# Kernel optimization log

Hardware: AMD Instinct MI355X
Metric: run time of the kernel (lower is better)

## Reference

```python
import jax, jax.numpy as jnp
import numpy as np

N_CLASSES = 19
N_BINS = 10
EPS = 1e-13


def setup_inputs() -> dict:
    key = jax.random.key(0)
    k1, k2 = jax.random.split(key)
    output = jax.random.normal(k1, (1, N_CLASSES, 1024, 2048), dtype=jnp.float32)
    target = jax.random.randint(k2, (1, 1024, 2048), 0, N_CLASSES, dtype=jnp.int32)
    return {"output": output, "target": target}


def reference(output, target):
    # output: [B, C, H, W] logits; target: [B, H, W] int labels
    B, C, H, W = output.shape
    p = jax.nn.softmax(output, axis=1)  # [B, C, H, W]

    # Bin i covers (i/N_BINS, (i+1)/N_BINS]; p == 0 belongs to no bin.
    bin_idx = jnp.clip(jnp.ceil(p * N_BINS).astype(jnp.int32) - 1, 0, N_BINS - 1)
    valid = p > 0

    cls = jnp.arange(C, dtype=jnp.int32)[None, :, None, None]  # idealMap per class
    # Combined (class, bin) segment id; invalid pixels dumped into extra segment.
    seg = jnp.where(valid, cls * N_BINS + bin_idx, C * N_BINS).reshape(-1)
    n_seg = C * N_BINS + 1

    p_flat = p.reshape(-1)
    conf_sum = jax.ops.segment_sum(p_flat, seg, num_segments=n_seg)[:-1].reshape(C, N_BINS)
    no_pred = jax.ops.segment_sum(jnp.ones_like(p_flat), seg, num_segments=n_seg)[:-1].reshape(C, N_BINS)
    correct = (target[:, None, :, :] == cls).astype(p.dtype)  # idealMap == target
    no_acc = jax.ops.segment_sum(correct.reshape(-1), seg, num_segments=n_seg)[:-1].reshape(C, N_BINS)

    avg_acc = no_acc / (no_pred + EPS)
    avg_conf = conf_sum / (no_pred + EPS)
    loss = jnp.sum((avg_acc - avg_conf) ** 2 * (no_pred / jnp.sum(no_pred)))
    return loss
```

## Files before the change

### kernel.cpp

```cpp
#include <hip/hip_runtime.h>

#define NC 19
#define NB 10
#define NCELL (NC * NB)
#define NPART (3 * NCELL + 2 * NC)
#define REP 4
#define NSLOT 16
#define BLOCKS 2048
#define TPB 256

__global__ __launch_bounds__(TPB) void cce_pass1(
    const float* __restrict__ logits, const int* __restrict__ tgt,
    float* __restrict__ gacc, int hw)
{
    constexpr int O_CONF = 0;
    constexpr int O_PRED = REP * NCELL;
    constexpr int O_ACC  = 2 * REP * NCELL;
    constexpr int O_PSUM = 3 * REP * NCELL;
    constexpr int O_INV  = 3 * REP * NCELL + REP * NC;
    constexpr int LDS_N  = O_INV + NC;

    __shared__ float lds[LDS_N];
    for (int i = threadIdx.x; i < LDS_N; i += TPB) lds[i] = 0.0f;
    __syncthreads();

    const int rep = threadIdx.x & (REP - 1);
    float psum[NC];
#pragma unroll
    for (int c = 0; c < NC; ++c) psum[c] = 0.0f;

    const int ngroups  = hw >> 1;
    const int tid      = blockIdx.x * TPB + threadIdx.x;
    const int nthreads = gridDim.x * TPB;

    for (int g = tid; g < ngroups; g += nthreads) {
        float xa[NC], xb[NC];
#pragma unroll
        for (int c = 0; c < NC; ++c) {
            const float2 v = *reinterpret_cast<const float2*>(
                logits + (size_t)c * hw + 2 * (size_t)g);
            xa[c] = v.x; xb[c] = v.y;
        }
        const int2 t2 = *reinterpret_cast<const int2*>(tgt + 2 * (size_t)g);

        float m0 = xa[0], m1 = xb[0];
#pragma unroll
        for (int c = 1; c < NC; ++c) { m0 = fmaxf(m0, xa[c]); m1 = fmaxf(m1, xb[c]); }

        float s0 = 0.0f, s1 = 0.0f;
#pragma unroll
        for (int c = 0; c < NC; ++c) {
            xa[c] = __expf(xa[c] - m0); s0 += xa[c];
            xb[c] = __expf(xb[c] - m1); s1 += xb[c];
        }
        const float r0 = __builtin_amdgcn_rcpf(s0);
        const float r1 = __builtin_amdgcn_rcpf(s1);

        float pt0 = 0.0f, pt1 = 0.0f, pmin0 = 1.0f, pmin1 = 1.0f;
#pragma unroll
        for (int c = 0; c < NC; ++c) {
            const float p0 = xa[c] * r0;
            const float p1 = xb[c] * r1;
            psum[c] += p0 + p1;
            if (c == t2.x) pt0 = p0;
            if (c == t2.y) pt1 = p1;
            pmin0 = fminf(pmin0, p0);
            pmin1 = fminf(pmin1, p1);
            const float q0 = p0 * 10.0f, q1 = p1 * 10.0f;
            if (q0 > 1.0f) {
                int b = (int)ceilf(q0) - 1; b = b > NB - 1 ? NB - 1 : b;
                atomicAdd(&lds[O_CONF + rep * NCELL + c * NB + b], p0);
                atomicAdd(&lds[O_PRED + rep * NCELL + c * NB + b], 1.0f);
            }
            if (q1 > 1.0f) {
                int b = (int)ceilf(q1) - 1; b = b > NB - 1 ? NB - 1 : b;
                atomicAdd(&lds[O_CONF + rep * NCELL + c * NB + b], p1);
                atomicAdd(&lds[O_PRED + rep * NCELL + c * NB + b], 1.0f);
            }
        }
        if (pt0 > 0.0f) {
            int b = (int)ceilf(pt0 * 10.0f) - 1;
            b = b < 0 ? 0 : (b > NB - 1 ? NB - 1 : b);
            atomicAdd(&lds[O_ACC + rep * NCELL + t2.x * NB + b], 1.0f);
        }
        if (pt1 > 0.0f) {
            int b = (int)ceilf(pt1 * 10.0f) - 1;
            b = b < 0 ? 0 : (b > NB - 1 ? NB - 1 : b);
            atomicAdd(&lds[O_ACC + rep * NCELL + t2.y * NB + b], 1.0f);
        }
        if (!(pmin0 > 0.0f)) {
#pragma unroll
            for (int c = 0; c < NC; ++c)
                if (!(xa[c] * r0 > 0.0f)) atomicAdd(&lds[O_INV + c], 1.0f);
        }
        if (!(pmin1 > 0.0f)) {
#pragma unroll
            for (int c = 0; c < NC; ++c)
                if (!(xb[c] * r1 > 0.0f)) atomicAdd(&lds[O_INV + c], 1.0f);
        }
    }
#pragma unroll
    for (int c = 0; c < NC; ++c)
        atomicAdd(&lds[O_PSUM + rep * NC + c], psum[c]);
    __syncthreads();

    float* slot = gacc + (size_t)(blockIdx.x & (NSLOT - 1)) * NPART;
    for (int j = threadIdx.x; j < NPART; j += TPB) {
        float v = 0.0f;
        if (j < NCELL) {
            for (int r = 0; r < REP; ++r) v += lds[O_CONF + r * NCELL + j];
        } else if (j < 2 * NCELL) {
            for (int r = 0; r < REP; ++r) v += lds[O_PRED + r * NCELL + (j - NCELL)];
        } else if (j < 3 * NCELL) {
            for (int r = 0; r < REP; ++r) v += lds[O_ACC + r * NCELL + (j - 2 * NCELL)];
        } else if (j < 3 * NCELL + NC) {
            for (int r = 0; r < REP; ++r) v += lds[O_PSUM + r * NC + (j - 3 * NCELL)];
        } else {
            v = lds[O_INV + (j - 3 * NCELL - NC)];
        }
        atomicAdd(&slot[j], v);
    }
}

__global__ void cce_pass2(const float* __restrict__ gacc, float* __restrict__ out, int hw)
{
    __shared__ double fin[NPART];
    const int j = threadIdx.x;
    if (j < NPART) {
        double v = 0.0;
        for (int s = 0; s < NSLOT; ++s) v += (double)gacc[(size_t)s * NPART + j];
        fin[j] = v;
    }
    __syncthreads();

    if (j < NC) {
        double spred = 0.0, sconf = 0.0;
        for (int b = 1; b < NB; ++b) {
            spred += fin[NCELL + j * NB + b];
            sconf += fin[j * NB + b];
        }
        const double validc = (double)hw - fin[3 * NCELL + NC + j];
        fin[NCELL + j * NB] = validc - spred;
        fin[j * NB]         = fin[3 * NCELL + j] - sconf;
    }
    __syncthreads();

    if (j < 64) {
        double tot = 0.0;
        for (int c = j; c < NCELL; c += 64) tot += fin[NCELL + c];
#pragma unroll
        for (int o = 32; o > 0; o >>= 1) tot += __shfl_down(tot, o);
        tot = __shfl(tot, 0);

        double loss = 0.0;
        for (int c = j; c < NCELL; c += 64) {
            const double pred = fin[NCELL + c];
            const double conf = fin[c];
            const double acc  = fin[2 * NCELL + c];
            const double d    = (acc - conf) / (pred + 1e-13);
            loss += d * d * (pred / tot);
        }
#pragma unroll
        for (int o = 32; o > 0; o >>= 1) loss += __shfl_down(loss, o);
        if (j == 0) out[0] = (float)loss;
    }
}

extern "C" void kernel_launch(void* const* d_in, const int* in_sizes, int n_in,
                              void* d_out, int out_size, void* d_ws, size_t ws_size,
                              hipStream_t stream)
{
    const float* logits = (const float*)d_in[0];
    const int*   tgt    = (const int*)d_in[1];
    float*       gacc   = (float*)d_ws;
    const int    hw     = in_sizes[1];

    hipMemsetAsync(gacc, 0, (size_t)NSLOT * NPART * sizeof(float), stream);
    cce_pass1<<<BLOCKS, TPB, 0, stream>>>(logits, tgt, gacc, hw);
    cce_pass2<<<1, 640, 0, stream>>>(gacc, (float*)d_out, hw);
}
```

Baseline: 296.2 us.

## Stage logit tiles into LDS with async global_load_lds double buffering

Pass 1 now processes 256-pixel tiles, with each block streaming the 19 logit rows plus the target row straight into a double-buffered LDS buffer through global_load_lds. The next tile's loads overlap compute on the current tile, and waits use vmcnt plus raw barriers. Each thread now handles one pixel per tile instead of two, and the grid shrinks to 768 blocks with launch bounds set for 3 blocks per CU. The aim is to hide HBM latency and cut register pressure. The cost is about 40KB of LDS per block, which limits occupancy, plus hand-written waitcnt logic that is fragile.

```diff
diff --git a/kernel.cpp b/kernel.cpp
--- a/kernel.cpp
+++ b/kernel.cpp
@@ -6,10 +6,20 @@
 #define NPART (3 * NCELL + 2 * NC)
 #define REP 4
 #define NSLOT 16
-#define BLOCKS 2048
 #define TPB 256
+#define TILE 256
+#define NROWS (NC + 1)
+#define BLOCKS 768
 
-__global__ __launch_bounds__(TPB) void cce_pass1(
+__device__ __forceinline__ void load16_lds(const void* g, void* l) {
+    auto* gp = reinterpret_cast<const unsigned int __attribute__((address_space(1)))*>(
+        reinterpret_cast<uintptr_t>(g));
+    auto* lp = reinterpret_cast<unsigned int __attribute__((address_space(3)))*>(
+        reinterpret_cast<uintptr_t>(l));
+    __builtin_amdgcn_global_load_lds(gp, lp, 16, 0, 0);
+}
+
+__global__ __launch_bounds__(TPB, 3) void cce_pass1(
     const float* __restrict__ logits, const int* __restrict__ tgt,
     float* __restrict__ gacc, int hw)
 {
@@ -20,103 +30,111 @@
     constexpr int O_INV  = 3 * REP * NCELL + REP * NC;
     constexpr int LDS_N  = O_INV + NC;
 
-    __shared__ float lds[LDS_N];
-    for (int i = threadIdx.x; i < LDS_N; i += TPB) lds[i] = 0.0f;
+    __shared__ float buf[2][NROWS][TILE];
+    __shared__ float hist[LDS_N];
+
+    for (int i = threadIdx.x; i < LDS_N; i += TPB) hist[i] = 0.0f;
     __syncthreads();
 
-    const int rep = threadIdx.x & (REP - 1);
+    const int lane = threadIdx.x & 63;
+    const int wv   = threadIdx.x >> 6;
+    const int rep  = threadIdx.x & (REP - 1);
+    const int p    = threadIdx.x;
+
     float psum[NC];
 #pragma unroll
     for (int c = 0; c < NC; ++c) psum[c] = 0.0f;
 
-    const int ngroups  = hw >> 1;
-    const int tid      = blockIdx.x * TPB + threadIdx.x;
-    const int nthreads = gridDim.x * TPB;
+    const int ntiles = hw / TILE;
+    const int stride = (int)gridDim.x;
 
-    for (int g = tid; g < ngroups; g += nthreads) {
-        float xa[NC], xb[NC];
+    auto stage = [&](int b, int t) {
+#pragma unroll
+        for (int r5 = 0; r5 < 5; ++r5) {
+            const int row = wv * 5 + r5;
+            const void* g = (row < NC)
+                ? (const void*)(logits + (size_t)row * hw + (size_t)t * TILE + lane * 4)
+                : (const void*)(tgt + (size_t)t * TILE + lane * 4);
+            load16_lds(g, (void*)&buf[b][row][0]);
+        }
+    };
+
+    const int t0 = (int)blockIdx.x;
+    if (t0 < ntiles) stage(0, t0);
+    int cur = 0;
+
+    for (int t = t0; t < ntiles; t += stride) {
+        const int nxt = t + stride;
+        if (nxt < ntiles) {
+            stage(cur ^ 1, nxt);
+            asm volatile("s_waitcnt vmcnt(5)" ::: "memory");
+        } else {
+            asm volatile("s_waitcnt vmcnt(0)" ::: "memory");
+        }
+        __builtin_amdgcn_s_barrier();
+        asm volatile("" ::: "memory");
+
+        float x[NC];
+#pragma unroll
+        for (int c = 0; c < NC; ++c) x[c] = buf[cur][c][p];
+        const int tg = ((const int*)&buf[cur][NC][0])[p];
+
+        float m = x[0];
+#pragma unroll
+        for (int c = 1; c < NC; ++c) m = fmaxf(m, x[c]);
+        float s = 0.0f;
+#pragma unroll
+        for (int c = 0; c < NC; ++c) { x[c] = __expf(x[c] - m); s += x[c]; }
+        const float r = __builtin_amdgcn_rcpf(s);
+
+        float pt = 0.0f, pmin = 1.0f;
 #pragma unroll
         for (int c = 0; c < NC; ++c) {
-            const float2 v = *reinterpret_cast<const float2*>(
-                logits + (size_t)c * hw + 2 * (size_t)g);
-            xa[c] = v.x; xb[c] = v.y;
-        }
-        const int2 t2 = *reinterpret_cast<const int2*>(tgt + 2 * (size_t)g);
-
-        float m0 = xa[0], m1 = xb[0];
-#pragma unroll
-        for (int c = 1; c < NC; ++c) { m0 = fmaxf(m0, xa[c]); m1 = fmaxf(m1, xb[c]); }
-
-        float s0 = 0.0f, s1 = 0.0f;
-#pragma unroll
-        for (int c = 0; c < NC; ++c) {
-            xa[c] = __expf(xa[c] - m0); s0 += xa[c];
-            xb[c] = __expf(xb[c] - m1); s1 += xb[c];
-        }
-        const float r0 = __builtin_amdgcn_rcpf(s0);
-        const float r1 = __builtin_amdgcn_rcpf(s1);
-
-        float pt0 = 0.0f, pt1 = 0.0f, pmin0 = 1.0f, pmin1 = 1.0f;
-#pragma unroll
-        for (int c = 0; c < NC; ++c) {
-            const float p0 = xa[c] * r0;
-            const float p1 = xb[c] * r1;
-            psum[c] += p0 + p1;
-            if (c == t2.x) pt0 = p0;
-            if (c == t2.y) pt1 = p1;
-            pmin0 = fminf(pmin0, p0);
-            pmin1 = fminf(pmin1, p1);
-            const float q0 = p0 * 10.0f, q1 = p1 * 10.0f;
-            if (q0 > 1.0f) {
-                int b = (int)ceilf(q0) - 1; b = b > NB - 1 ? NB - 1 : b;
-                atomicAdd(&lds[O_CONF + rep * NCELL + c * NB + b], p0);
-                atomicAdd(&lds[O_PRED + rep * NCELL + c * NB + b], 1.0f);
-            }
-            if (q1 > 1.0f) {
-                int b = (int)ceilf(q1) - 1; b = b > NB - 1 ? NB - 1 : b;
-                atomicAdd(&lds[O_CONF + rep * NCELL + c * NB + b], p1);
-                atomicAdd(&lds[O_PRED + rep * NCELL + c * NB + b], 1.0f);
+            const float pv = x[c] * r;
+            psum[c] += pv;
+            if (c == tg) pt = pv;
+            pmin = fminf(pmin, pv);
+            const float q = pv * 10.0f;
+            if (q > 1.0f) {
+                int bb = (int)ceilf(q) - 1; bb = bb > NB - 1 ? NB - 1 : bb;
+                atomicAdd(&hist[O_CONF + rep * NCELL + c * NB + bb], pv);
+                atomicAdd(&hist[O_PRED + rep * NCELL + c * NB + bb], 1.0f);
             }
         }
-        if (pt0 > 0.0f) {
-            int b = (int)ceilf(pt0 * 10.0f) - 1;
-            b = b < 0 ? 0 : (b > NB - 1 ? NB - 1 : b);
-            atomicAdd(&lds[O_ACC + rep * NCELL + t2.x * NB + b], 1.0f);
+        if (pt > 0.0f) {
+            int bb = (int)ceilf(pt * 10.0f) - 1;
+            bb = bb < 0 ? 0 : (bb > NB - 1 ? NB - 1 : bb);
+            atomicAdd(&hist[O_ACC + rep * NCELL + tg * NB + bb], 1.0f);
         }
-        if (pt1 > 0.0f) {
-            int b = (int)ceilf(pt1 * 10.0f) - 1;
-            b = b < 0 ? 0 : (b > NB - 1 ? NB - 1 : b);
-            atomicAdd(&lds[O_ACC + rep * NCELL + t2.y * NB + b], 1.0f);
-        }
-        if (!(pmin0 > 0.0f)) {
+        if (!(pmin > 0.0f)) {
 #pragma unroll
             for (int c = 0; c < NC; ++c)
-                if (!(xa[c] * r0 > 0.0f)) atomicAdd(&lds[O_INV + c], 1.0f);
+                if (!(x[c] * r > 0.0f)) atomicAdd(&hist[O_INV + c], 1.0f);
         }
-        if (!(pmin1 > 0.0f)) {
-#pragma unroll
-            for (int c = 0; c < NC; ++c)
-                if (!(xb[c] * r1 > 0.0f)) atomicAdd(&lds[O_INV + c], 1.0f);
-        }
+
+        asm volatile("" ::: "memory");
+        __builtin_amdgcn_s_barrier();
+        cur ^= 1;
     }
+
 #pragma unroll
     for (int c = 0; c < NC; ++c)
-        atomicAdd(&lds[O_PSUM + rep * NC + c], psum[c]);
+        atomicAdd(&hist[O_PSUM + rep * NC + c], psum[c]);
     __syncthreads();
 
     float* slot = gacc + (size_t)(blockIdx.x & (NSLOT - 1)) * NPART;
     for (int j = threadIdx.x; j < NPART; j += TPB) {
         float v = 0.0f;
         if (j < NCELL) {
-            for (int r = 0; r < REP; ++r) v += lds[O_CONF + r * NCELL + j];
+            for (int rr = 0; rr < REP; ++rr) v += hist[O_CONF + rr * NCELL + j];
         } else if (j < 2 * NCELL) {
-            for (int r = 0; r < REP; ++r) v += lds[O_PRED + r * NCELL + (j - NCELL)];
+            for (int rr = 0; rr < REP; ++rr) v += hist[O_PRED + rr * NCELL + (j - NCELL)];
         } else if (j < 3 * NCELL) {
-            for (int r = 0; r < REP; ++r) v += lds[O_ACC + r * NCELL + (j - 2 * NCELL)];
+            for (int rr = 0; rr < REP; ++rr) v += hist[O_ACC + rr * NCELL + (j - 2 * NCELL)];
         } else if (j < 3 * NCELL + NC) {
-            for (int r = 0; r < REP; ++r) v += lds[O_PSUM + r * NC + (j - 3 * NCELL)];
+            for (int rr = 0; rr < REP; ++rr) v += hist[O_PSUM + rr * NC + (j - 3 * NCELL)];
         } else {
-            v = lds[O_INV + (j - 3 * NCELL - NC)];
+            v = hist[O_INV + (j - 3 * NCELL - NC)];
         }
         atomicAdd(&slot[j], v);
     }
```

New measurement: 271.6 us. 1.09x faster.
